# Optimization experiments

Measured on AMD Instinct MI355X. Metric: run time of the kernel, lower is better.

Reference implementation:

```python
import jax, jax.numpy as jnp
import numpy as np

IMAGE_W = 640
IMAGE_H = 640
SCALE = jnp.array([0.1, 0.1, 0.2, 0.2], dtype=jnp.float32)
TOP_N = 1000
MIN_SCORE = 0.05
NMS_THR = 0.5
MAX_DET = 100


def setup_inputs() -> dict:
    key = jax.random.key(0)
    kc, kr, k1, k2 = jax.random.split(key, 4)
    B, A, C = 8, 120000, 80
    cls_heads = jax.random.uniform(kc, (B, A, C), dtype=jnp.float32)  # sigmoid-like scores
    reg_heads = jax.random.normal(kr, (B, A, 4), dtype=jnp.float32)
    # valid anchors: centers inside image, wh in [16, 256]
    ctr = jax.random.uniform(k1, (B, A, 2), minval=0.0, maxval=640.0, dtype=jnp.float32)
    wh = jax.random.uniform(k2, (B, A, 2), minval=16.0, maxval=256.0, dtype=jnp.float32)
    batch_anchors = jnp.concatenate([ctr - 0.5 * wh, ctr + 0.5 * wh], axis=-1)
    return {"cls_heads": cls_heads, "reg_heads": reg_heads, "batch_anchors": batch_anchors}


def _decode(reg, anchors):
    # reg: [N,4] (tx,ty,tw,th), anchors: [N,4] (x1,y1,x2,y2)
    awh = anchors[:, 2:] - anchors[:, :2]
    actr = anchors[:, :2] + 0.5 * awh
    reg = reg * SCALE
    pwh = jnp.exp(reg[:, 2:]) * awh
    pctr = reg[:, :2] * awh + actr
    boxes = jnp.concatenate([pctr - 0.5 * pwh, pctr + 0.5 * pwh], axis=1)
    boxes = jnp.trunc(boxes)  # mimics torch .int() truncation
    boxes = jnp.stack([
        jnp.maximum(boxes[:, 0], 0.0),
        jnp.maximum(boxes[:, 1], 0.0),
        jnp.minimum(boxes[:, 2], float(IMAGE_W - 1)),
        jnp.minimum(boxes[:, 3], float(IMAGE_H - 1)),
    ], axis=1)
    return boxes


def _nms_image(scores, classes, boxes):
    # scores sorted descending (from top_k); class-agnostic greedy NMS.
    N = scores.shape[0]
    valid = scores > MIN_SCORE
    area = (boxes[:, 2] - boxes[:, 0]) * (boxes[:, 3] - boxes[:, 1])
    lt = jnp.maximum(boxes[:, None, :2], boxes[None, :, :2])
    rb = jnp.minimum(boxes[:, None, 2:], boxes[None, :, 2:])
    inter = jnp.prod(jnp.clip(rb - lt, 0.0, None), axis=-1)  # [N,N]
    iou = inter / (area[:, None] + area[None, :] - inter)
    idx = jnp.arange(N)

    def body(i, keep):
        supp = (iou[i] > NMS_THR) & (idx > i) & keep[i]
        return keep & ~supp

    keep = jax.lax.fori_loop(0, N, body, valid)
    order = jnp.argsort(~keep, stable=True)  # kept first, score order preserved
    take = order[:MAX_DET]
    n_keep = jnp.sum(keep)
    slot = jnp.arange(MAX_DET) < n_keep
    out_s = jnp.where(slot, scores[take], -1.0)
    out_c = jnp.where(slot, classes[take].astype(jnp.float32), -1.0)
    out_b = jnp.where(slot[:, None], boxes[take], -1.0)
    return out_s, out_c, out_b


def reference(cls_heads, reg_heads, batch_anchors):
    # per-anchor best class
    scores0 = jnp.max(cls_heads, axis=2)          # [B,A]
    classes0 = jnp.argmax(cls_heads, axis=2)      # [B,A]
    top_scores, top_idx = jax.lax.top_k(scores0, TOP_N)  # sorted descending
    top_classes = jnp.take_along_axis(classes0, top_idx, axis=1)
    top_reg = jnp.take_along_axis(reg_heads, top_idx[..., None], axis=1)
    top_anchors = jnp.take_along_axis(batch_anchors, top_idx[..., None], axis=1)

    def per_image(s, c, r, a):
        boxes = _decode(r, a)
        return _nms_image(s, c, boxes)

    batch_scores, batch_classes, batch_bboxes = jax.vmap(per_image)(
        top_scores, top_classes, top_reg, top_anchors)
    return batch_scores, batch_classes, batch_bboxes
```

## Files before the change

### kernel.cpp

```cpp
#include <hip/hip_runtime.h>
#include <math.h>

#define AN 120000
#define NB 8
#define NC 80
#define TOPN 1000
#define MAXDET 100
#define CAND_CAP 2048
#define CAND_T 0.99985f

typedef unsigned long long u64;
typedef unsigned int u32;

__device__ __forceinline__ float opaquef(float x) { asm volatile("" : "+v"(x)); return x; }

__global__ __launch_bounds__(256) void score_kernel(const float* __restrict__ cls,
                                                    u64* __restrict__ keys,
                                                    int* __restrict__ cls_out,
                                                    u64* __restrict__ cand,
                                                    u32* __restrict__ cand_cnt) {
    __shared__ float buf[4][32 * 81];
    const int tid = threadIdx.x;
    const int wave = tid >> 6, lane = tid & 63;
    const long long blockbase = (long long)blockIdx.x * 256;

    for (int h = 0; h < 2; ++h) {
        const long long abase = blockbase + wave * 64 + h * 32;
        const float4* src = (const float4*)(cls + abase * NC);
        float* Bf = buf[wave];
#pragma unroll
        for (int it = 0; it < 10; ++it) {
            int f = lane + it * 64;
            float4 v = src[f];
            int anch = f / 20, pos = (f % 20) * 4;
            float* dst = Bf + anch * 81 + pos;
            dst[0] = v.x; dst[1] = v.y; dst[2] = v.z; dst[3] = v.w;
        }
        __syncthreads();
        int anch = lane >> 1, half = lane & 1;
        const float* row = Bf + anch * 81 + half * 40;
        float best = -1.0f; int bi = 0;
#pragma unroll
        for (int i = 0; i < 40; ++i) {
            float v = row[i];
            if (v > best) { best = v; bi = i; }
        }
        bi += half * 40;
        float ov = __shfl_xor(best, 1);
        int   oi = __shfl_xor(bi, 1);
        if (ov > best || (ov == best && oi < bi)) { best = ov; bi = oi; }
        if (half == 0) {
            long long aglob = abase + anch;
            int a = (int)(aglob % AN);
            u64 key = ((u64)__float_as_uint(best) << 17) | (u64)(131071 - a);
            keys[aglob]    = key;
            cls_out[aglob] = bi;
            if (best >= CAND_T) {
                int im = (int)(aglob / AN);
                u32 p = atomicAdd(&cand_cnt[im], 1u);
                if (p < CAND_CAP) cand[(size_t)im * CAND_CAP + p] = key;
            }
        }
        __syncthreads();
    }
}

__global__ __launch_bounds__(1024) void topk_nms_kernel(const u64* __restrict__ keys,
                                                        const u64* __restrict__ cand,
                                                        const u32* __restrict__ cand_cnt,
                                                        const int* __restrict__ clsin,
                                                        const float* __restrict__ reg,
                                                        const float* __restrict__ anch,
                                                        float* __restrict__ out) {
    const int img = blockIdx.x;
    const int tid = threadIdx.x;

    __shared__ u64 stopk[CAND_CAP];
    __shared__ float4 sbox[TOPN];
    __shared__ u32 hist[256];
    __shared__ u32 sscan[256];
    __shared__ float ssc[TOPN];
    __shared__ int   scl[TOPN];
    __shared__ int keeplist[MAXDET];
    __shared__ int s_nkeep;
    __shared__ u32 s_need, s_digit, s_cnt;
    __shared__ u64 s_prefix;

    const u32 cnt = cand_cnt[img];
    if (cnt >= (u32)TOPN && cnt <= (u32)CAND_CAP) {
        const u64* c = cand + (size_t)img * CAND_CAP;
        for (int i = tid; i < CAND_CAP; i += 1024)
            stopk[i] = (i < (int)cnt) ? ~c[i] : ~0ull;
        __syncthreads();
        for (int kk = 2; kk <= CAND_CAP; kk <<= 1) {
            for (int j = kk >> 1; j > 0; j >>= 1) {
                for (int i = tid; i < CAND_CAP; i += 1024) {
                    int ixj = i ^ j;
                    if (ixj > i) {
                        u64 a = stopk[i], b = stopk[ixj];
                        bool asc = ((i & kk) == 0);
                        if ((a > b) == asc) { stopk[i] = b; stopk[ixj] = a; }
                    }
                }
                __syncthreads();
            }
        }
    } else {
        const u64* k = keys + (size_t)img * AN;
        if (tid == 0) { s_need = TOPN; s_prefix = 0; s_cnt = 0; }
        stopk[tid] = ~0ull;
        __syncthreads();

        for (int lvl = 0; lvl < 6; ++lvl) {
            const int shift = 40 - 8 * lvl;
            if (tid < 256) hist[tid] = 0;
            __syncthreads();
            const u64 P = s_prefix;
            const u32 need = s_need;
            for (int i = tid; i < AN; i += 1024) {
                u64 K = k[i];
                if ((K >> (shift + 8)) == P)
                    atomicAdd(&hist[(u32)((K >> shift) & 255)], 1u);
            }
            __syncthreads();
            if (tid < 256) sscan[tid] = hist[tid];
            __syncthreads();
            for (int off = 1; off < 256; off <<= 1) {
                u32 v = 0;
                if (tid < 256 && tid + off < 256) v = sscan[tid + off];
                __syncthreads();
                if (tid < 256) sscan[tid] += v;
                __syncthreads();
            }
            if (tid < 256) {
                u32 above = (tid == 255) ? 0u : sscan[tid + 1];
                if (sscan[tid] >= need && above < need) {
                    s_digit = (u32)tid;
                    s_need = need - above;
                }
            }
            __syncthreads();
            if (tid == 0) s_prefix = (s_prefix << 8) | (u64)s_digit;
            __syncthreads();
        }

        const u64 T = s_prefix;
        for (int i = tid; i < AN; i += 1024) {
            u64 K = k[i];
            if (K >= T) {
                u32 pos = atomicAdd(&s_cnt, 1u);
                if (pos < 1024) stopk[pos] = ~K;
            }
        }
        __syncthreads();
        for (int kk = 2; kk <= 1024; kk <<= 1) {
            for (int j = kk >> 1; j > 0; j >>= 1) {
                int ixj = tid ^ j;
                if (ixj > tid) {
                    u64 a = stopk[tid], b = stopk[ixj];
                    bool asc = ((tid & kk) == 0);
                    if ((a > b) == asc) { stopk[tid] = b; stopk[ixj] = a; }
                }
                __syncthreads();
            }
        }
    }

    if (tid < TOPN) {
        u64 K = ~stopk[tid];
        u32 sb = (u32)(K >> 17);
        int idx = 131071 - (int)(K & 0x1FFFF);
        float score = __uint_as_float(sb);
        size_t gi = (size_t)img * AN + idx;

        float4 r = ((const float4*)reg)[gi];
        float4 a = ((const float4*)anch)[gi];

        float aw = a.z - a.x, ah = a.w - a.y;
        float acx = a.x + 0.5f * aw, acy = a.y + 0.5f * ah;
        float rx = opaquef(r.x * 0.1f), ry = opaquef(r.y * 0.1f);
        float rw = opaquef(r.z * 0.2f), rh = opaquef(r.w * 0.2f);
        float pw = opaquef((float)exp((double)rw) * aw);
        float ph = opaquef((float)exp((double)rh) * ah);
        float pcx = opaquef(rx * aw) + acx;
        float pcy = opaquef(ry * ah) + acy;
        float x1 = truncf(pcx - 0.5f * pw);
        float y1 = truncf(pcy - 0.5f * ph);
        float x2 = truncf(pcx + 0.5f * pw);
        float y2 = truncf(pcy + 0.5f * ph);
        x1 = fmaxf(x1, 0.0f); y1 = fmaxf(y1, 0.0f);
        x2 = fminf(x2, 639.0f); y2 = fminf(y2, 639.0f);

        sbox[tid] = make_float4(x1, y1, x2, y2);
        ssc[tid]  = score;
        scl[tid]  = clsin[gi];
    }
    __syncthreads();

    if (tid < 64) {
        const int lane = tid;
        float4 bj[16]; float aj[16];
#pragma unroll
        for (int w = 0; w < 16; ++w) {
            int j = w * 64 + lane;
            float4 b = (j < TOPN) ? sbox[j] : make_float4(0.f, 0.f, 0.f, 0.f);
            bj[w] = b;
            aj[w] = (b.z - b.x) * (b.w - b.y);
        }
        u32 pmask = 0;
        int kept = 0;
        for (int i = 0; i < TOPN; ++i) {
            u32 pm = __shfl(pmask, i & 63);
            bool removed = (pm >> (i >> 6)) & 1u;
            float sc = ssc[i];
            float4 bi = sbox[i];
            if (sc > 0.05f && !removed) {
                if (lane == 0) keeplist[kept] = i;
                kept++;
                if (kept >= MAXDET) break;
                float ai = (bi.z - bi.x) * (bi.w - bi.y);
#pragma unroll
                for (int w = 0; w < 16; ++w) {
                    int j = w * 64 + lane;
                    float ltx = fmaxf(bi.x, bj[w].x), lty = fmaxf(bi.y, bj[w].y);
                    float rbx = fminf(bi.z, bj[w].z), rby = fminf(bi.w, bj[w].w);
                    float dx = fmaxf(rbx - ltx, 0.0f), dy = fmaxf(rby - lty, 0.0f);
                    float inter = dx * dy;
                    float uni = ai + aj[w] - inter;
                    bool p = (j < TOPN) && (j > i) && ((inter / uni) > 0.5f);
                    pmask |= p ? (1u << w) : 0u;
                }
            }
        }
        if (lane == 0) s_nkeep = kept;
    }
    __syncthreads();

    if (tid < MAXDET) {
        int o = img * MAXDET + tid;
        if (tid < s_nkeep) {
            int i = keeplist[tid];
            out[o] = ssc[i];
            out[NB * MAXDET + o] = (float)scl[i];
            ((float4*)(out + 2 * NB * MAXDET))[o] = sbox[i];
        } else {
            out[o] = -1.0f;
            out[NB * MAXDET + o] = -1.0f;
            ((float4*)(out + 2 * NB * MAXDET))[o] = make_float4(-1.f, -1.f, -1.f, -1.f);
        }
    }
}

extern "C" void kernel_launch(void* const* d_in, const int* in_sizes, int n_in,
                              void* d_out, int out_size, void* d_ws, size_t ws_size,
                              hipStream_t stream) {
    const float* cls  = (const float*)d_in[0];
    const float* reg  = (const float*)d_in[1];
    const float* anch = (const float*)d_in[2];
    float* out = (float*)d_out;

    u64* keys   = (u64*)d_ws;
    u64* cand   = keys + (size_t)NB * AN;
    int* clsmax = (int*)(cand + (size_t)NB * CAND_CAP);
    u32* ccnt   = (u32*)(clsmax + (size_t)NB * AN);

    hipMemsetAsync(ccnt, 0, NB * sizeof(u32), stream);
    hipLaunchKernelGGL(score_kernel,    dim3(3750), dim3(256),  0, stream, cls, keys, clsmax, cand, ccnt);
    hipLaunchKernelGGL(topk_nms_kernel, dim3(NB),   dim3(1024), 0, stream, keys, cand, ccnt, clsmax, reg, anch, out);
}
```

Baseline: 626.5 us.

## Skip suppressed candidates in NMS using per-chunk wave ballots

Rewrites the greedy NMS loop so it walks 64-candidate chunks. A ballot finds the surviving, above-threshold candidates in each chunk, and the loop jumps straight to the next survivor with ctz instead of visiting all 1000 indices serially. After each kept box, a ballot of its suppression predicate for the current chunk updates the active mask. This removes the per-index shuffle and shared-memory loads for suppressed or low-score entries. In exchange it adds 16 ballots per kept box.

```diff
diff --git a/kernel.cpp b/kernel.cpp
--- a/kernel.cpp
+++ b/kernel.cpp
@@ -200,36 +200,44 @@
     if (tid < 64) {
         const int lane = tid;
         float4 bj[16]; float aj[16];
+        u32 scok = 0;
 #pragma unroll
         for (int w = 0; w < 16; ++w) {
             int j = w * 64 + lane;
             float4 b = (j < TOPN) ? sbox[j] : make_float4(0.f, 0.f, 0.f, 0.f);
             bj[w] = b;
             aj[w] = (b.z - b.x) * (b.w - b.y);
+            bool ok = (j < TOPN) && (ssc[j] > 0.05f);
+            scok |= (ok ? 1u : 0u) << w;
         }
         u32 pmask = 0;
         int kept = 0;
-        for (int i = 0; i < TOPN; ++i) {
-            u32 pm = __shfl(pmask, i & 63);
-            bool removed = (pm >> (i >> 6)) & 1u;
-            float sc = ssc[i];
-            float4 bi = sbox[i];
-            if (sc > 0.05f && !removed) {
+        for (int w = 0; w < 16 && kept < MAXDET; ++w) {
+            u64 aw_ = __ballot(((scok >> w) & 1u) && !((pmask >> w) & 1u));
+            while (aw_) {
+                int b = __builtin_ctzll(aw_);
+                int i = w * 64 + b;
                 if (lane == 0) keeplist[kept] = i;
                 kept++;
                 if (kept >= MAXDET) break;
+                float4 bi = sbox[i];
                 float ai = (bi.z - bi.x) * (bi.w - bi.y);
-#pragma unroll
-                for (int w = 0; w < 16; ++w) {
-                    int j = w * 64 + lane;
-                    float ltx = fmaxf(bi.x, bj[w].x), lty = fmaxf(bi.y, bj[w].y);
-                    float rbx = fminf(bi.z, bj[w].z), rby = fminf(bi.w, bj[w].w);
+                u64 mcur = 0;
+#pragma unroll
+                for (int w2 = 0; w2 < 16; ++w2) {
+                    int j = w2 * 64 + lane;
+                    float ltx = fmaxf(bi.x, bj[w2].x), lty = fmaxf(bi.y, bj[w2].y);
+                    float rbx = fminf(bi.z, bj[w2].z), rby = fminf(bi.w, bj[w2].w);
                     float dx = fmaxf(rbx - ltx, 0.0f), dy = fmaxf(rby - lty, 0.0f);
                     float inter = dx * dy;
-                    float uni = ai + aj[w] - inter;
+                    float uni = ai + aj[w2] - inter;
                     bool p = (j < TOPN) && (j > i) && ((inter / uni) > 0.5f);
-                    pmask |= p ? (1u << w) : 0u;
-                }
+                    pmask |= (p ? 1u : 0u) << w2;
+                    u64 m = __ballot(p);
+                    if (w2 == w) mcur = m;
+                }
+                aw_ &= ~mcur;
+                aw_ &= (b < 63) ? (~0ull << (b + 1)) : 0ull;
             }
         }
         if (lane == 0) s_nkeep = kept;
```

Result: no change. 631.0 us (+0.7%).
